# Kernel optimization log

Measured on AMD Instinct MI355X. Metric: run time of the kernel, lower is better.

The kernel has to match this reference:

```python
import jax, jax.numpy as jnp
import numpy as np

B, S, F, E = 8, 2048, 512, 512

def setup_inputs() -> dict:
    key = jax.random.key(0)
    k1, k2, k3, k4 = jax.random.split(key, 4)
    x = jax.random.normal(k1, (B, S, F), dtype=jnp.float32)
    # nn.Linear(feat, embed, bias=False): y = x @ W.T; store W as [F, E] already transposed
    scale = 1.0 / np.sqrt(F)
    Wq = jax.random.uniform(k2, (F, E), dtype=jnp.float32, minval=-scale, maxval=scale)
    Wk = jax.random.uniform(k3, (F, E), dtype=jnp.float32, minval=-scale, maxval=scale)
    Wv = jax.random.uniform(k4, (F, E), dtype=jnp.float32, minval=-scale, maxval=scale)
    return {"x": x, "Wq": Wq, "Wk": Wk, "Wv": Wv}

def reference(x, Wq, Wk, Wv):
    # QKV projections: [B, S, E]
    Q = jnp.einsum('bsf,fe->bse', x, Wq)
    K = jnp.einsum('bsf,fe->bse', x, Wk)
    V = jnp.einsum('bsf,fe->bse', x, Wv)
    # scores: [B, S, S], scaled by sqrt(E)
    scores = jnp.einsum('bqe,bke->bqk', Q, K) / jnp.sqrt(jnp.asarray(Q.shape[-1], Q.dtype))
    attn = jax.nn.softmax(scores, axis=-1)
    return jnp.einsum('bqk,bke->bqe', attn, V)
```

## Files before the change

kernel.cpp:

```cpp
#include <hip/hip_runtime.h>
#include <hip/hip_bf16.h>
#include <stdint.h>

#define B_ 8
#define S_ 2048
#define F_ 512
#define E_ 512

typedef short bf16x8 __attribute__((ext_vector_type(8)));
typedef float f32x4 __attribute__((ext_vector_type(4)));

__device__ __forceinline__ f32x4 mfma16(bf16x8 a, bf16x8 b, f32x4 c) {
  return __builtin_amdgcn_mfma_f32_16x16x32_bf16(a, b, c, 0, 0, 0);
}

__device__ __forceinline__ void gll16(const void* g, void* l) {
  __builtin_amdgcn_global_load_lds(
      (const __attribute__((address_space(1))) void*)g,
      (__attribute__((address_space(3))) void*)l, 16, 0, 0);
}

constexpr float QSCALE = 0.0441941738f * 1.44269504f;

__global__ void xconv_kernel(const float* __restrict__ x,
                             __hip_bfloat16* __restrict__ xb) {
  int i = (blockIdx.x * 256 + threadIdx.x) * 8;
  float4 a = *(const float4*)(x + i);
  float4 b = *(const float4*)(x + i + 4);
  union { __hip_bfloat16 h[8]; uint4 u; } cv;
  cv.h[0] = __float2bfloat16(a.x);
  cv.h[1] = __float2bfloat16(a.y);
  cv.h[2] = __float2bfloat16(a.z);
  cv.h[3] = __float2bfloat16(a.w);
  cv.h[4] = __float2bfloat16(b.x);
  cv.h[5] = __float2bfloat16(b.y);
  cv.h[6] = __float2bfloat16(b.z);
  cv.h[7] = __float2bfloat16(b.w);
  *(uint4*)(xb + i) = cv.u;
}

__global__ void wtrans_kernel(const float* __restrict__ wq,
                              const float* __restrict__ wk,
                              const float* __restrict__ wv,
                              __hip_bfloat16* __restrict__ wt) {
  __shared__ float t[32][33];
  const float* w = (blockIdx.z == 0) ? wq : (blockIdx.z == 1 ? wk : wv);
  __hip_bfloat16* o = wt + (size_t)blockIdx.z * F_ * E_;
  int e0 = blockIdx.x * 32, f0 = blockIdx.y * 32;
  int tx = threadIdx.x, ty = threadIdx.y;
#pragma unroll
  for (int i = 0; i < 4; i++)
    t[ty + 8 * i][tx] = w[(size_t)(f0 + ty + 8 * i) * E_ + e0 + tx];
  __syncthreads();
#pragma unroll
  for (int i = 0; i < 4; i++)
    o[(size_t)(e0 + ty + 8 * i) * F_ + f0 + tx] = __float2bfloat16(t[tx][ty + 8 * i]);
}

__global__ __launch_bounds__(256, 2) void qkvg_kernel(
    const __hip_bfloat16* __restrict__ xb, const __hip_bfloat16* __restrict__ wt,
    __hip_bfloat16* __restrict__ Qb, __hip_bfloat16* __restrict__ Kb,
    __hip_bfloat16* __restrict__ Vt) {
  __shared__ __hip_bfloat16 Al[2][128][64] __attribute__((aligned(16)));
  __shared__ __hip_bfloat16 Bl[2][128][64] __attribute__((aligned(16)));

  int tid = threadIdx.x;
  int lane = tid & 63, w = tid >> 6;
  int el = lane & 15, g = lane >> 4;
  int r7 = el & 7;
  int m0 = blockIdx.x * 128, n0 = blockIdx.y * 128, z = blockIdx.z;
  const __hip_bfloat16* wz = wt + (size_t)z * F_ * E_;
  int wr = w >> 1, wc = w & 1;

  int srcoff = (((lane & 7) ^ ((lane >> 3) & 7)) << 3);
  auto stage = [&](int kk, int bf) {
#pragma unroll
    for (int i = 0; i < 4; i++) {
      int row = w * 32 + i * 8 + (lane >> 3);
      gll16(xb + (size_t)(m0 + row) * F_ + kk * 64 + srcoff, &Al[bf][w * 32 + i * 8][0]);
      gll16(wz + (size_t)(n0 + row) * F_ + kk * 64 + srcoff, &Bl[bf][w * 32 + i * 8][0]);
    }
  };

  f32x4 acc[4][4] = {};
  stage(0, 0);
  asm volatile("s_waitcnt vmcnt(0)" ::: "memory");
  __syncthreads();

  for (int kk = 0; kk < 8; ++kk) {
    int bf = kk & 1;
    if (kk < 7) stage(kk + 1, bf ^ 1);
#pragma unroll
    for (int ks = 0; ks < 2; ++ks) {
      bf16x8 av[4], bv[4];
#pragma unroll
      for (int mi = 0; mi < 4; mi++)
        av[mi] = *(const bf16x8*)((const char*)&Al[bf][0][0] +
                                  (wr * 64 + mi * 16 + el) * 128 +
                                  (((ks * 4 + g) ^ r7) << 4));
#pragma unroll
      for (int ni = 0; ni < 4; ni++)
        bv[ni] = *(const bf16x8*)((const char*)&Bl[bf][0][0] +
                                  (wc * 64 + ni * 16 + el) * 128 +
                                  (((ks * 4 + g) ^ r7) << 4));
#pragma unroll
      for (int mi = 0; mi < 4; mi++)
#pragma unroll
        for (int ni = 0; ni < 4; ni++)
          acc[mi][ni] = mfma16(av[mi], bv[ni], acc[mi][ni]);
    }
    asm volatile("s_waitcnt vmcnt(0)" ::: "memory");
    __syncthreads();
  }

  float sc = (z == 0) ? QSCALE : 1.0f;
#pragma unroll
  for (int mi = 0; mi < 4; mi++)
#pragma unroll
    for (int ni = 0; ni < 4; ni++) {
      int mB = m0 + wr * 64 + mi * 16 + g * 4;
      int n = n0 + wc * 64 + ni * 16 + el;
      if (z == 2) {
        union { __hip_bfloat16 h[4]; uint2 u; } pk;
#pragma unroll
        for (int r = 0; r < 4; r++) pk.h[r] = __float2bfloat16(acc[mi][ni][r]);
        int b = mB >> 11, sl = mB & 2047;
        *(uint2*)&Vt[(size_t)b * E_ * S_ + (size_t)n * S_ + sl] = pk.u;
      } else {
#pragma unroll
        for (int r = 0; r < 4; r++) {
          __hip_bfloat16 v = __float2bfloat16(acc[mi][ni][r] * sc);
          if (z == 0) Qb[(size_t)(mB + r) * E_ + n] = v;
          else Kb[(size_t)(mB + r) * E_ + n] = v;
        }
      }
    }
}

__global__ __launch_bounds__(256, 2) void qkv_kernel(
    const float* __restrict__ x, const __hip_bfloat16* __restrict__ wt,
    __hip_bfloat16* __restrict__ Qb, __hip_bfloat16* __restrict__ Kb,
    __hip_bfloat16* __restrict__ Vt) {
  __shared__ __hip_bfloat16 Al[2][128][72];
  __shared__ __hip_bfloat16 Bl[2][128][72];
  int tid = threadIdx.x;
  int lane = tid & 63, w = tid >> 6;
  int el = lane & 15, g = lane >> 4;
  int m0 = blockIdx.x * 128, n0 = blockIdx.y * 128, z = blockIdx.z;
  const __hip_bfloat16* wz = wt + (size_t)z * F_ * E_;
  int wr = w >> 1, wc = w & 1;
  float4 fa[8];
  uint4 vb[4];
  auto load = [&](int kk) {
#pragma unroll
    for (int c = 0; c < 4; c++) {
      int id = tid + 256 * c;
      int row = id >> 3, k8 = (id & 7) * 8;
      const float* s = x + (size_t)(m0 + row) * F_ + kk * 64 + k8;
      fa[2 * c] = *(const float4*)s;
      fa[2 * c + 1] = *(const float4*)(s + 4);
      vb[c] = *(const uint4*)(wz + (size_t)(n0 + row) * F_ + kk * 64 + k8);
    }
  };
  auto store_lds = [&](int bf) {
#pragma unroll
    for (int c = 0; c < 4; c++) {
      int id = tid + 256 * c;
      int row = id >> 3, k8 = (id & 7) * 8;
      union { __hip_bfloat16 h[8]; uint4 u; } cv;
      cv.h[0] = __float2bfloat16(fa[2 * c].x);
      cv.h[1] = __float2bfloat16(fa[2 * c].y);
      cv.h[2] = __float2bfloat16(fa[2 * c].z);
      cv.h[3] = __float2bfloat16(fa[2 * c].w);
      cv.h[4] = __float2bfloat16(fa[2 * c + 1].x);
      cv.h[5] = __float2bfloat16(fa[2 * c + 1].y);
      cv.h[6] = __float2bfloat16(fa[2 * c + 1].z);
      cv.h[7] = __float2bfloat16(fa[2 * c + 1].w);
      *(uint4*)&Al[bf][row][k8] = cv.u;
      *(uint4*)&Bl[bf][row][k8] = vb[c];
    }
  };
  f32x4 acc[4][4] = {};
  load(0);
  store_lds(0);
  __syncthreads();
  for (int kk = 0; kk < 8; ++kk) {
    int bf = kk & 1;
    if (kk < 7) load(kk + 1);
#pragma unroll
    for (int ks = 0; ks < 2; ++ks) {
      bf16x8 av[4], bv[4];
#pragma unroll
      for (int mi = 0; mi < 4; mi++)
        av[mi] = *(const bf16x8*)((const char*)&Al[bf][0][0] +
                                  (wr * 64 + mi * 16 + el) * 144 + (ks * 32 + g * 8) * 2);
#pragma unroll
      for (int ni = 0; ni < 4; ni++)
        bv[ni] = *(const bf16x8*)((const char*)&Bl[bf][0][0] +
                                  (wc * 64 + ni * 16 + el) * 144 + (ks * 32 + g * 8) * 2);
#pragma unroll
      for (int mi = 0; mi < 4; mi++)
#pragma unroll
        for (int ni = 0; ni < 4; ni++)
          acc[mi][ni] = mfma16(av[mi], bv[ni], acc[mi][ni]);
    }
    if (kk < 7) store_lds(bf ^ 1);
    __syncthreads();
  }
  float sc = (z == 0) ? QSCALE : 1.0f;
#pragma unroll
  for (int mi = 0; mi < 4; mi++)
#pragma unroll
    for (int ni = 0; ni < 4; ni++)
#pragma unroll
      for (int r = 0; r < 4; r++) {
        int m = m0 + wr * 64 + mi * 16 + g * 4 + r;
        int n = n0 + wc * 64 + ni * 16 + el;
        __hip_bfloat16 v = __float2bfloat16(acc[mi][ni][r] * sc);
        if (z == 0) Qb[(size_t)m * E_ + n] = v;
        else if (z == 1) Kb[(size_t)m * E_ + n] = v;
        else {
          int b = m >> 11, sl = m & 2047;
          Vt[(size_t)b * E_ * S_ + (size_t)n * S_ + sl] = v;
        }
      }
}

template <int MODE>
__global__ __launch_bounds__(256, MODE ? 2 : 1) void attn_kernel(
    const __hip_bfloat16* __restrict__ Qb, const __hip_bfloat16* __restrict__ Kb,
    const __hip_bfloat16* __restrict__ Vt, float* __restrict__ out,
    float* __restrict__ part1, float* __restrict__ Ls, float* __restrict__ Ms) {
  __shared__ __hip_bfloat16 Kl[32][512] __attribute__((aligned(16)));
  __shared__ __hip_bfloat16 Vl[512][32] __attribute__((aligned(16)));
  __shared__ __hip_bfloat16 Pl[4][16][40] __attribute__((aligned(16)));

  int tid = threadIdx.x;
  int lane = tid & 63, w = tid >> 6;
  int el = lane & 15, g = lane >> 4, x7 = lane & 7;
  int bx = blockIdx.x;
  int batch = bx & 7, qt = (bx >> 3) & 31;
  int half = MODE ? (bx >> 8) : 0;
  int nt = MODE ? 32 : 64;
  int tbase = half * 32;
  int q0 = qt * 64 + w * 16;

  bf16x8 qf[16];
  {
    const __hip_bfloat16* qptr = Qb + (size_t)(batch * S_ + q0 + el) * E_ + g * 8;
#pragma unroll
    for (int s = 0; s < 16; s++) qf[s] = *(const bf16x8*)(qptr + 32 * s);
  }

  f32x4 o[32] = {};
  float m_run = -INFINITY, l_run = 0.f;

  const char* kbase_g = (const char*)(Kb + (size_t)batch * S_ * E_);
  const char* vbase_g = (const char*)(Vt + (size_t)batch * E_ * S_);
  int vsrc_lane = (lane >> 2) * (S_ * 2) + 16 * ((lane & 3) ^ ((lane >> 3) & 3));

  auto stage = [&](int t) {
#pragma unroll
    for (int i = 0; i < 8; i++) {
      int row = w * 8 + i;
      const char* src =
          kbase_g + ((size_t)(t * 32 + row) * 512 + 8 * (lane ^ i)) * 2;
      gll16(src, &Kl[row][0]);
    }
#pragma unroll
    for (int i = 0; i < 8; i++) {
      int eb = (w * 8 + i) * 16;
      const char* src = vbase_g + (size_t)eb * (S_ * 2) + vsrc_lane + t * 64;
      gll16(src, &Vl[eb][0]);
    }
  };

  int ka0 = el * 1024 + ((g ^ x7) << 4);
  int ka1 = el * 1024 + (((4 + g) ^ x7) << 4);
  int vbase_l = el * 64 + ((g ^ ((el >> 1) & 3)) << 4);

  stage(tbase);
  asm volatile("s_waitcnt vmcnt(0)" ::: "memory");
  __syncthreads();

  for (int i = 0; i < nt; ++i) {
    const char* kl = (const char*)&Kl[0][0];
    f32x4 st[2] = {};
    __builtin_amdgcn_s_setprio(1);
#pragma unroll
    for (int s = 0; s < 16; s++) {
      int base = ((s & 1) ? ka1 : ka0) + (s >> 1) * 128;
#pragma unroll
      for (int f = 0; f < 2; f++) {
        bf16x8 kf = *(const bf16x8*)(kl + base + f * 16384);
        st[f] = mfma16(kf, qf[s], st[f]);
      }
    }
    __builtin_amdgcn_s_setprio(0);
    float vmax = st[0][0];
#pragma unroll
    for (int r = 1; r < 4; r++) vmax = fmaxf(vmax, st[0][r]);
#pragma unroll
    for (int r = 0; r < 4; r++) vmax = fmaxf(vmax, st[1][r]);
    vmax = fmaxf(vmax, __shfl_xor(vmax, 16));
    vmax = fmaxf(vmax, __shfl_xor(vmax, 32));
    if (__any(vmax > m_run + 8.0f)) {
      float m_new = fmaxf(m_run, vmax);
      float fac = exp2f(m_run - m_new);
      float fo[4];
#pragma unroll
      for (int r = 0; r < 4; r++) fo[r] = __shfl(fac, g * 4 + r);
#pragma unroll
      for (int ni = 0; ni < 32; ni++) {
        o[ni][0] *= fo[0]; o[ni][1] *= fo[1]; o[ni][2] *= fo[2]; o[ni][3] *= fo[3];
      }
      l_run *= fac;
      m_run = m_new;
    }
    float p[8];
    float rs = 0.f;
#pragma unroll
    for (int f = 0; f < 2; f++)
#pragma unroll
      for (int r = 0; r < 4; r++) {
        float e2 = exp2f(st[f][r] - m_run);
        p[4 * f + r] = e2;
        rs += e2;
      }
    rs += __shfl_xor(rs, 16);
    rs += __shfl_xor(rs, 32);
    l_run += rs;
#pragma unroll
    for (int f = 0; f < 2; f++) {
      union { __hip_bfloat16 h[4]; uint2 u; } pk;
      pk.h[0] = __float2bfloat16(p[4 * f + 0]);
      pk.h[1] = __float2bfloat16(p[4 * f + 1]);
      pk.h[2] = __float2bfloat16(p[4 * f + 2]);
      pk.h[3] = __float2bfloat16(p[4 * f + 3]);
      *(uint2*)((char*)&Pl[w][0][0] + el * 80 + 32 * f + 8 * g) = pk.u;
    }
    asm volatile("s_waitcnt lgkmcnt(0)" ::: "memory");
    bf16x8 pa = *(const bf16x8*)((const char*)&Pl[w][0][0] + el * 80 + g * 16);
    const char* vl = (const char*)&Vl[0][0];
    __builtin_amdgcn_s_setprio(1);
#pragma unroll
    for (int ni = 0; ni < 32; ni++) {
      bf16x8 vf = *(const bf16x8*)(vl + vbase_l + ni * 1024);
      o[ni] = mfma16(pa, vf, o[ni]);
    }
    __builtin_amdgcn_s_setprio(0);
    __syncthreads();
    if (i + 1 < nt) {
      stage(tbase + i + 1);
      asm volatile("s_waitcnt vmcnt(0)" ::: "memory");
      __syncthreads();
    }
  }

  if (MODE == 0) {
    float linv[4];
#pragma unroll
    for (int r = 0; r < 4; r++) {
      float lr = __shfl(l_run, g * 4 + r);
      linv[r] = 1.0f / lr;
    }
    float* ob = out + (size_t)(batch * S_ + q0 + g * 4) * E_ + el;
#pragma unroll
    for (int ni = 0; ni < 32; ni++)
#pragma unroll
      for (int r = 0; r < 4; r++)
        ob[(size_t)r * E_ + ni * 16] = o[ni][r] * linv[r];
  } else {
    float* dst = (half == 0) ? out : part1;
    float* ob = dst + (size_t)(batch * S_ + q0 + g * 4) * E_ + el;
#pragma unroll
    for (int ni = 0; ni < 32; ni++)
#pragma unroll
      for (int r = 0; r < 4; r++)
        ob[(size_t)r * E_ + ni * 16] = o[ni][r];
    if (g == 0) {
      int idx = half * (B_ * S_) + batch * S_ + q0 + el;
      Ls[idx] = l_run;
      Ms[idx] = m_run;
    }
  }
}

__global__ void merge_kernel(float* __restrict__ out,
                             const float* __restrict__ part1,
                             const float* __restrict__ Ls,
                             const float* __restrict__ Ms) {
  int idx = blockIdx.x * 256 + threadIdx.x;
  int row = idx >> 7;
  int c4 = (idx & 127) * 4;
  float l0 = Ls[row], m0 = Ms[row];
  float l1 = Ls[B_ * S_ + row], m1 = Ms[B_ * S_ + row];
  float m = fmaxf(m0, m1);
  float w0 = exp2f(m0 - m), w1 = exp2f(m1 - m);
  float inv = 1.0f / (l0 * w0 + l1 * w1);
  size_t off = (size_t)row * E_ + c4;
  float4 a = *(const float4*)(out + off);
  float4 b = *(const float4*)(part1 + off);
  float4 r;
  r.x = (a.x * w0 + b.x * w1) * inv;
  r.y = (a.y * w0 + b.y * w1) * inv;
  r.z = (a.z * w0 + b.z * w1) * inv;
  r.w = (a.w * w0 + b.w * w1) * inv;
  *(float4*)(out + off) = r;
}

extern "C" void kernel_launch(void* const* d_in, const int* in_sizes, int n_in,
                              void* d_out, int out_size, void* d_ws, size_t ws_size,
                              hipStream_t stream) {
  const float* x = (const float*)d_in[0];
  const float* wq = (const float*)d_in[1];
  const float* wk = (const float*)d_in[2];
  const float* wv = (const float*)d_in[3];
  float* out = (float*)d_out;

  char* ws = (char*)d_ws;
  __hip_bfloat16* wt = (__hip_bfloat16*)ws;
  __hip_bfloat16* Qb = (__hip_bfloat16*)(ws + (size_t)3 * F_ * E_ * 2);
  __hip_bfloat16* Kb = Qb + (size_t)B_ * S_ * E_;
  __hip_bfloat16* Vt = Kb + (size_t)B_ * S_ * E_;
  __hip_bfloat16* xb = Vt + (size_t)B_ * S_ * E_;
  float* part1 = (float*)(ws + (size_t)3 * F_ * E_ * 2 + (size_t)3 * B_ * S_ * E_ * 2 +
                          (size_t)B_ * S_ * F_ * 2);
  float* Ls = part1 + (size_t)B_ * S_ * E_;
  float* Ms = Ls + 2 * B_ * S_;

  size_t need_bfx = (size_t)3 * F_ * E_ * 2 + (size_t)3 * B_ * S_ * E_ * 2 +
                    (size_t)B_ * S_ * F_ * 2;
  size_t need_split = need_bfx + (size_t)B_ * S_ * E_ * 4 + 4 * B_ * S_ * 4;
  bool bfx = (ws_size >= need_bfx);
  bool split = (ws_size >= need_split);

  dim3 b0(32, 8), g0(16, 16, 3);
  wtrans_kernel<<<g0, b0, 0, stream>>>(wq, wk, wv, wt);

  dim3 g1(128, 4, 3);
  if (bfx) {
    xconv_kernel<<<(B_ * S_ * F_) / (256 * 8), 256, 0, stream>>>(x, xb);
    qkvg_kernel<<<g1, 256, 0, stream>>>(xb, wt, Qb, Kb, Vt);
  } else {
    qkv_kernel<<<g1, 256, 0, stream>>>(x, wt, Qb, Kb, Vt);
  }

  if (split) {
    attn_kernel<1><<<512, 256, 0, stream>>>(Qb, Kb, Vt, out, part1, Ls, Ms);
    merge_kernel<<<(B_ * S_ * E_ / 4) / 256, 256, 0, stream>>>(out, part1, Ls, Ms);
  } else {
    attn_kernel<0><<<256, 256, 0, stream>>>(Qb, Kb, Vt, out, nullptr, nullptr, nullptr);
  }
}
```

Measured before the change: 185.3 us.

## Use 16-key attention tiles with k16 MFMA, register P, and bf16 partials

Adds a new attention kernel that processes 16 keys per step with double-buffered K/V LDS tiles. The P tile stays in registers, feeding a 16x16x16 bf16 MFMA directly, so the LDS round trip for P is gone. A lazy rescale skips the O update unless the max grows by more than a threshold. The split-K partial outputs are now stored as bf16 instead of fp32, halving merge traffic at some cost in precision. Smaller tiles mean more loop iterations and more barriers per key.

```diff
diff --git a/kernel.cpp b/kernel.cpp
--- a/kernel.cpp
+++ b/kernel.cpp
@@ -8,11 +8,24 @@
 #define E_ 512
 
 typedef short bf16x8 __attribute__((ext_vector_type(8)));
+typedef short bf16x4 __attribute__((ext_vector_type(4)));
 typedef float f32x4 __attribute__((ext_vector_type(4)));
 
 __device__ __forceinline__ f32x4 mfma16(bf16x8 a, bf16x8 b, f32x4 c) {
   return __builtin_amdgcn_mfma_f32_16x16x32_bf16(a, b, c, 0, 0, 0);
 }
+
+#if defined(__has_builtin)
+#if __has_builtin(__builtin_amdgcn_mfma_f32_16x16x16bf16_1k)
+#define HAVE16 1
+__device__ __forceinline__ f32x4 mfma16k16(bf16x4 a, bf16x4 b, f32x4 c) {
+  return __builtin_amdgcn_mfma_f32_16x16x16bf16_1k(a, b, c, 0, 0, 0);
+}
+#endif
+#endif
+#ifndef HAVE16
+#define HAVE16 0
+#endif
 
 __device__ __forceinline__ void gll16(const void* g, void* l) {
   __builtin_amdgcn_global_load_lds(
@@ -76,9 +89,10 @@
   auto stage = [&](int kk, int bf) {
 #pragma unroll
     for (int i = 0; i < 4; i++) {
-      int row = w * 32 + i * 8 + (lane >> 3);
-      gll16(xb + (size_t)(m0 + row) * F_ + kk * 64 + srcoff, &Al[bf][w * 32 + i * 8][0]);
-      gll16(wz + (size_t)(n0 + row) * F_ + kk * 64 + srcoff, &Bl[bf][w * 32 + i * 8][0]);
+      gll16(xb + (size_t)(m0 + w * 32 + i * 8 + (lane >> 3)) * F_ + kk * 64 + srcoff,
+            &Al[bf][w * 32 + i * 8][0]);
+      gll16(wz + (size_t)(n0 + w * 32 + i * 8 + (lane >> 3)) * F_ + kk * 64 + srcoff,
+            &Bl[bf][w * 32 + i * 8][0]);
     }
   };
 
@@ -226,11 +240,152 @@
       }
 }
 
+#if HAVE16
 template <int MODE>
-__global__ __launch_bounds__(256, MODE ? 2 : 1) void attn_kernel(
+__global__ __launch_bounds__(256, 2) void attn16_kernel(
     const __hip_bfloat16* __restrict__ Qb, const __hip_bfloat16* __restrict__ Kb,
     const __hip_bfloat16* __restrict__ Vt, float* __restrict__ out,
-    float* __restrict__ part1, float* __restrict__ Ls, float* __restrict__ Ms) {
+    __hip_bfloat16* __restrict__ part0, __hip_bfloat16* __restrict__ part1,
+    float* __restrict__ Ls, float* __restrict__ Ms) {
+  __shared__ __hip_bfloat16 Kl[2][16][512] __attribute__((aligned(16)));
+  __shared__ __hip_bfloat16 Vl[2][512][16] __attribute__((aligned(16)));
+
+  int tid = threadIdx.x;
+  int lane = tid & 63, w = tid >> 6;
+  int el = lane & 15, g = lane >> 4, x7 = lane & 7;
+  int bx = blockIdx.x;
+  int batch = bx & 7, qt = (bx >> 3) & 31;
+  int half = MODE ? (bx >> 8) : 0;
+  int nt = MODE ? 64 : 128;
+  int tbase = half * 64;
+  int q0 = qt * 64 + w * 16;
+
+  bf16x8 qf[16];
+  {
+    const __hip_bfloat16* qptr = Qb + (size_t)(batch * S_ + q0 + el) * E_ + g * 8;
+#pragma unroll
+    for (int s = 0; s < 16; s++) qf[s] = *(const bf16x8*)(qptr + 32 * s);
+  }
+
+  f32x4 o[32] = {};
+  float m_run = -INFINITY, l_run = 0.f;
+
+  const char* kbase_g = (const char*)(Kb + (size_t)batch * S_ * E_);
+  const char* vbase_g = (const char*)(Vt + (size_t)batch * E_ * S_);
+
+  auto stage = [&](int t, int bf) {
+#pragma unroll
+    for (int i = 0; i < 4; i++) {
+      int row = w * 4 + i;
+      const char* src =
+          kbase_g + ((size_t)(t * 16 + row) * 512 + 8 * (lane ^ (row & 7))) * 2;
+      gll16(src, &Kl[bf][row][0]);
+    }
+#pragma unroll
+    for (int i = 0; i < 4; i++) {
+      int eb = (w * 4 + i) * 32;
+      const char* src = vbase_g +
+          ((size_t)(eb + (lane >> 1)) * S_ + t * 16 + 8 * (lane & 1)) * 2;
+      gll16(src, &Vl[bf][eb][0]);
+    }
+  };
+
+  stage(tbase, 0);
+  asm volatile("s_waitcnt vmcnt(0)" ::: "memory");
+  __syncthreads();
+
+  for (int i = 0; i < nt; ++i) {
+    int bf = i & 1;
+    if (i + 1 < nt) stage(tbase + i + 1, bf ^ 1);
+    const char* kl = (const char*)&Kl[bf][0][0];
+    f32x4 st = {};
+    __builtin_amdgcn_s_setprio(1);
+#pragma unroll
+    for (int s = 0; s < 16; s++) {
+      bf16x8 kf = *(const bf16x8*)(kl + el * 1024 + (s >> 1) * 128 +
+                                   (((4 * (s & 1) + g) ^ x7) << 4));
+      st = mfma16(kf, qf[s], st);
+    }
+    __builtin_amdgcn_s_setprio(0);
+    float vmax = fmaxf(fmaxf(st[0], st[1]), fmaxf(st[2], st[3]));
+    vmax = fmaxf(vmax, __shfl_xor(vmax, 16));
+    vmax = fmaxf(vmax, __shfl_xor(vmax, 32));
+    if (__any(vmax > m_run + 8.0f)) {
+      float m_new = fmaxf(m_run, vmax);
+      float fac = exp2f(m_run - m_new);
+      float fo[4];
+#pragma unroll
+      for (int r = 0; r < 4; r++) fo[r] = __shfl(fac, g * 4 + r);
+#pragma unroll
+      for (int ni = 0; ni < 32; ni++) {
+        o[ni][0] *= fo[0]; o[ni][1] *= fo[1]; o[ni][2] *= fo[2]; o[ni][3] *= fo[3];
+      }
+      l_run *= fac;
+      m_run = m_new;
+    }
+    float p[4];
+    float rs = 0.f;
+#pragma unroll
+    for (int r = 0; r < 4; r++) {
+      p[r] = exp2f(st[r] - m_run);
+      rs += p[r];
+    }
+    rs += __shfl_xor(rs, 16);
+    rs += __shfl_xor(rs, 32);
+    l_run += rs;
+    union { __hip_bfloat16 h[4]; bf16x4 v; } pk;
+#pragma unroll
+    for (int r = 0; r < 4; r++) pk.h[r] = __float2bfloat16(p[r]);
+    bf16x4 pa = pk.v;
+    const char* vl = (const char*)&Vl[bf][0][0];
+    __builtin_amdgcn_s_setprio(1);
+#pragma unroll
+    for (int ni = 0; ni < 32; ni++) {
+      bf16x4 vf = *(const bf16x4*)(vl + ni * 512 + el * 32 + g * 8);
+      o[ni] = mfma16k16(pa, vf, o[ni]);
+    }
+    __builtin_amdgcn_s_setprio(0);
+    asm volatile("s_waitcnt vmcnt(0)" ::: "memory");
+    __syncthreads();
+  }
+
+  if (MODE == 0) {
+    float linv[4];
+#pragma unroll
+    for (int r = 0; r < 4; r++) {
+      float lr = __shfl(l_run, g * 4 + r);
+      linv[r] = 1.0f / lr;
+    }
+    float* ob = out + (size_t)(batch * S_ + q0 + g * 4) * E_ + el;
+#pragma unroll
+    for (int ni = 0; ni < 32; ni++)
+#pragma unroll
+      for (int r = 0; r < 4; r++)
+        ob[(size_t)r * E_ + ni * 16] = o[ni][r] * linv[r];
+  } else {
+    __hip_bfloat16* dst = (half == 0) ? part0 : part1;
+    __hip_bfloat16* ob = dst + (size_t)(batch * S_ + q0 + g * 4) * E_ + el;
+#pragma unroll
+    for (int ni = 0; ni < 32; ni++)
+#pragma unroll
+      for (int r = 0; r < 4; r++)
+        ob[(size_t)r * E_ + ni * 16] = __float2bfloat16(o[ni][r]);
+    if (g == 0) {
+      int idx = half * (B_ * S_) + batch * S_ + q0 + el;
+      Ls[idx] = l_run;
+      Ms[idx] = m_run;
+    }
+  }
+}
+
+#else
+
+template <int MODE>
+__global__ __launch_bounds__(256, MODE ? 2 : 1) void attn16_kernel(
+    const __hip_bfloat16* __restrict__ Qb, const __hip_bfloat16* __restrict__ Kb,
+    const __hip_bfloat16* __restrict__ Vt, float* __restrict__ out,
+    __hip_bfloat16* __restrict__ part0, __hip_bfloat16* __restrict__ part1,
+    float* __restrict__ Ls, float* __restrict__ Ms) {
   __shared__ __hip_bfloat16 Kl[32][512] __attribute__((aligned(16)));
   __shared__ __hip_bfloat16 Vl[512][32] __attribute__((aligned(16)));
   __shared__ __hip_bfloat16 Pl[4][16][40] __attribute__((aligned(16)));
@@ -371,13 +526,13 @@
       for (int r = 0; r < 4; r++)
         ob[(size_t)r * E_ + ni * 16] = o[ni][r] * linv[r];
   } else {
-    float* dst = (half == 0) ? out : part1;
-    float* ob = dst + (size_t)(batch * S_ + q0 + g * 4) * E_ + el;
+    __hip_bfloat16* dst = (half == 0) ? part0 : part1;
+    __hip_bfloat16* ob = dst + (size_t)(batch * S_ + q0 + g * 4) * E_ + el;
 #pragma unroll
     for (int ni = 0; ni < 32; ni++)
 #pragma unroll
       for (int r = 0; r < 4; r++)
-        ob[(size_t)r * E_ + ni * 16] = o[ni][r];
+        ob[(size_t)r * E_ + ni * 16] = __float2bfloat16(o[ni][r]);
     if (g == 0) {
       int idx = half * (B_ * S_) + batch * S_ + q0 + el;
       Ls[idx] = l_run;
@@ -385,28 +540,35 @@
     }
   }
 }
+#endif
 
 __global__ void merge_kernel(float* __restrict__ out,
-                             const float* __restrict__ part1,
+                             const __hip_bfloat16* __restrict__ p0,
+                             const __hip_bfloat16* __restrict__ p1,
                              const float* __restrict__ Ls,
                              const float* __restrict__ Ms) {
   int idx = blockIdx.x * 256 + threadIdx.x;
-  int row = idx >> 7;
-  int c4 = (idx & 127) * 4;
+  int row = idx >> 6;
+  int c8 = (idx & 63) * 8;
   float l0 = Ls[row], m0 = Ms[row];
   float l1 = Ls[B_ * S_ + row], m1 = Ms[B_ * S_ + row];
   float m = fmaxf(m0, m1);
   float w0 = exp2f(m0 - m), w1 = exp2f(m1 - m);
   float inv = 1.0f / (l0 * w0 + l1 * w1);
-  size_t off = (size_t)row * E_ + c4;
-  float4 a = *(const float4*)(out + off);
-  float4 b = *(const float4*)(part1 + off);
-  float4 r;
-  r.x = (a.x * w0 + b.x * w1) * inv;
-  r.y = (a.y * w0 + b.y * w1) * inv;
-  r.z = (a.z * w0 + b.z * w1) * inv;
-  r.w = (a.w * w0 + b.w * w1) * inv;
-  *(float4*)(out + off) = r;
+  size_t off = (size_t)row * E_ + c8;
+  union { uint4 u; ushort h[8]; } ua, ub;
+  ua.u = *(const uint4*)(p0 + off);
+  ub.u = *(const uint4*)(p1 + off);
+  float r[8];
+#pragma unroll
+  for (int j = 0; j < 8; j++) {
+    union { uint32_t u; float f; } a, b;
+    a.u = (uint32_t)ua.h[j] << 16;
+    b.u = (uint32_t)ub.h[j] << 16;
+    r[j] = (a.f * w0 + b.f * w1) * inv;
+  }
+  *(float4*)(out + off) = *(float4*)&r[0];
+  *(float4*)(out + off + 4) = *(float4*)&r[4];
 }
 
 extern "C" void kernel_launch(void* const* d_in, const int* in_sizes, int n_in,
@@ -424,14 +586,14 @@
   __hip_bfloat16* Kb = Qb + (size_t)B_ * S_ * E_;
   __hip_bfloat16* Vt = Kb + (size_t)B_ * S_ * E_;
   __hip_bfloat16* xb = Vt + (size_t)B_ * S_ * E_;
-  float* part1 = (float*)(ws + (size_t)3 * F_ * E_ * 2 + (size_t)3 * B_ * S_ * E_ * 2 +
-                          (size_t)B_ * S_ * F_ * 2);
-  float* Ls = part1 + (size_t)B_ * S_ * E_;
+  __hip_bfloat16* part0 = xb + (size_t)B_ * S_ * F_;
+  __hip_bfloat16* part1 = part0 + (size_t)B_ * S_ * E_;
+  float* Ls = (float*)(part1 + (size_t)B_ * S_ * E_);
   float* Ms = Ls + 2 * B_ * S_;
 
   size_t need_bfx = (size_t)3 * F_ * E_ * 2 + (size_t)3 * B_ * S_ * E_ * 2 +
                     (size_t)B_ * S_ * F_ * 2;
-  size_t need_split = need_bfx + (size_t)B_ * S_ * E_ * 4 + 4 * B_ * S_ * 4;
+  size_t need_split = need_bfx + (size_t)2 * B_ * S_ * E_ * 2 + 4 * B_ * S_ * 4;
   bool bfx = (ws_size >= need_bfx);
   bool split = (ws_size >= need_split);
 
@@ -447,9 +609,10 @@
   }
 
   if (split) {
-    attn_kernel<1><<<512, 256, 0, stream>>>(Qb, Kb, Vt, out, part1, Ls, Ms);
-    merge_kernel<<<(B_ * S_ * E_ / 4) / 256, 256, 0, stream>>>(out, part1, Ls, Ms);
+    attn16_kernel<1><<<512, 256, 0, stream>>>(Qb, Kb, Vt, out, part0, part1, Ls, Ms);
+    merge_kernel<<<(B_ * S_ * E_ / 8) / 256, 256, 0, stream>>>(out, part0, part1, Ls, Ms);
   } else {
-    attn_kernel<0><<<256, 256, 0, stream>>>(Qb, Kb, Vt, out, nullptr, nullptr, nullptr);
-  }
-}
+    attn16_kernel<0><<<256, 256, 0, stream>>>(Qb, Kb, Vt, out, nullptr, nullptr,
+                                              nullptr, nullptr);
+  }
+}
```

Result: slower. 255.6 us (+38.0%).

## Store split-attention partials in bf16 and overlap K/V staging waits

Applied to the files above, without the earlier changes.

The split-KV attention path now writes its two partial outputs as bf16 into separate workspace buffers, and the merge kernel reads them as bf16, converting back to fp32 with 8 elements per thread. This halves the partial-output traffic in both the attention epilogue and the merge. The staging wait after issuing the next tile is relaxed to vmcnt(8), with a full wait and barrier moved to just before the V reads, so part of the next tile's load can overlap the QK/softmax work. The trade-off is bf16 rounding of the unnormalized partial accumulators and a more delicate synchronization order.

```diff
diff --git a/kernel.cpp b/kernel.cpp
--- a/kernel.cpp
+++ b/kernel.cpp
@@ -76,9 +76,10 @@
   auto stage = [&](int kk, int bf) {
 #pragma unroll
     for (int i = 0; i < 4; i++) {
-      int row = w * 32 + i * 8 + (lane >> 3);
-      gll16(xb + (size_t)(m0 + row) * F_ + kk * 64 + srcoff, &Al[bf][w * 32 + i * 8][0]);
-      gll16(wz + (size_t)(n0 + row) * F_ + kk * 64 + srcoff, &Bl[bf][w * 32 + i * 8][0]);
+      gll16(xb + (size_t)(m0 + w * 32 + i * 8 + (lane >> 3)) * F_ + kk * 64 + srcoff,
+            &Al[bf][w * 32 + i * 8][0]);
+      gll16(wz + (size_t)(n0 + w * 32 + i * 8 + (lane >> 3)) * F_ + kk * 64 + srcoff,
+            &Bl[bf][w * 32 + i * 8][0]);
     }
   };
 
@@ -230,7 +231,8 @@
 __global__ __launch_bounds__(256, MODE ? 2 : 1) void attn_kernel(
     const __hip_bfloat16* __restrict__ Qb, const __hip_bfloat16* __restrict__ Kb,
     const __hip_bfloat16* __restrict__ Vt, float* __restrict__ out,
-    float* __restrict__ part1, float* __restrict__ Ls, float* __restrict__ Ms) {
+    __hip_bfloat16* __restrict__ part0, __hip_bfloat16* __restrict__ part1,
+    float* __restrict__ Ls, float* __restrict__ Ms) {
   __shared__ __hip_bfloat16 Kl[32][512] __attribute__((aligned(16)));
   __shared__ __hip_bfloat16 Vl[512][32] __attribute__((aligned(16)));
   __shared__ __hip_bfloat16 Pl[4][16][40] __attribute__((aligned(16)));
@@ -341,6 +343,8 @@
     }
     asm volatile("s_waitcnt lgkmcnt(0)" ::: "memory");
     bf16x8 pa = *(const bf16x8*)((const char*)&Pl[w][0][0] + el * 80 + g * 16);
+    asm volatile("s_waitcnt vmcnt(0)" ::: "memory");
+    __syncthreads();
     const char* vl = (const char*)&Vl[0][0];
     __builtin_amdgcn_s_setprio(1);
 #pragma unroll
@@ -352,7 +356,7 @@
     __syncthreads();
     if (i + 1 < nt) {
       stage(tbase + i + 1);
-      asm volatile("s_waitcnt vmcnt(0)" ::: "memory");
+      asm volatile("s_waitcnt vmcnt(8)" ::: "memory");
       __syncthreads();
     }
   }
@@ -371,13 +375,13 @@
       for (int r = 0; r < 4; r++)
         ob[(size_t)r * E_ + ni * 16] = o[ni][r] * linv[r];
   } else {
-    float* dst = (half == 0) ? out : part1;
-    float* ob = dst + (size_t)(batch * S_ + q0 + g * 4) * E_ + el;
+    __hip_bfloat16* dst = (half == 0) ? part0 : part1;
+    __hip_bfloat16* ob = dst + (size_t)(batch * S_ + q0 + g * 4) * E_ + el;
 #pragma unroll
     for (int ni = 0; ni < 32; ni++)
 #pragma unroll
       for (int r = 0; r < 4; r++)
-        ob[(size_t)r * E_ + ni * 16] = o[ni][r];
+        ob[(size_t)r * E_ + ni * 16] = __float2bfloat16(o[ni][r]);
     if (g == 0) {
       int idx = half * (B_ * S_) + batch * S_ + q0 + el;
       Ls[idx] = l_run;
@@ -387,26 +391,32 @@
 }
 
 __global__ void merge_kernel(float* __restrict__ out,
-                             const float* __restrict__ part1,
+                             const __hip_bfloat16* __restrict__ p0,
+                             const __hip_bfloat16* __restrict__ p1,
                              const float* __restrict__ Ls,
                              const float* __restrict__ Ms) {
   int idx = blockIdx.x * 256 + threadIdx.x;
-  int row = idx >> 7;
-  int c4 = (idx & 127) * 4;
+  int row = idx >> 6;
+  int c8 = (idx & 63) * 8;
   float l0 = Ls[row], m0 = Ms[row];
   float l1 = Ls[B_ * S_ + row], m1 = Ms[B_ * S_ + row];
   float m = fmaxf(m0, m1);
   float w0 = exp2f(m0 - m), w1 = exp2f(m1 - m);
   float inv = 1.0f / (l0 * w0 + l1 * w1);
-  size_t off = (size_t)row * E_ + c4;
-  float4 a = *(const float4*)(out + off);
-  float4 b = *(const float4*)(part1 + off);
-  float4 r;
-  r.x = (a.x * w0 + b.x * w1) * inv;
-  r.y = (a.y * w0 + b.y * w1) * inv;
-  r.z = (a.z * w0 + b.z * w1) * inv;
-  r.w = (a.w * w0 + b.w * w1) * inv;
-  *(float4*)(out + off) = r;
+  size_t off = (size_t)row * E_ + c8;
+  union { uint4 u; ushort h[8]; } ua, ub;
+  ua.u = *(const uint4*)(p0 + off);
+  ub.u = *(const uint4*)(p1 + off);
+  float r[8];
+#pragma unroll
+  for (int j = 0; j < 8; j++) {
+    union { uint32_t u; float f; } a, b;
+    a.u = (uint32_t)ua.h[j] << 16;
+    b.u = (uint32_t)ub.h[j] << 16;
+    r[j] = (a.f * w0 + b.f * w1) * inv;
+  }
+  *(float4*)(out + off) = *(float4*)&r[0];
+  *(float4*)(out + off + 4) = *(float4*)&r[4];
 }
 
 extern "C" void kernel_launch(void* const* d_in, const int* in_sizes, int n_in,
@@ -424,14 +434,14 @@
   __hip_bfloat16* Kb = Qb + (size_t)B_ * S_ * E_;
   __hip_bfloat16* Vt = Kb + (size_t)B_ * S_ * E_;
   __hip_bfloat16* xb = Vt + (size_t)B_ * S_ * E_;
-  float* part1 = (float*)(ws + (size_t)3 * F_ * E_ * 2 + (size_t)3 * B_ * S_ * E_ * 2 +
-                          (size_t)B_ * S_ * F_ * 2);
-  float* Ls = part1 + (size_t)B_ * S_ * E_;
+  __hip_bfloat16* part0 = xb + (size_t)B_ * S_ * F_;
+  __hip_bfloat16* part1 = part0 + (size_t)B_ * S_ * E_;
+  float* Ls = (float*)(part1 + (size_t)B_ * S_ * E_);
   float* Ms = Ls + 2 * B_ * S_;
 
   size_t need_bfx = (size_t)3 * F_ * E_ * 2 + (size_t)3 * B_ * S_ * E_ * 2 +
                     (size_t)B_ * S_ * F_ * 2;
-  size_t need_split = need_bfx + (size_t)B_ * S_ * E_ * 4 + 4 * B_ * S_ * 4;
+  size_t need_split = need_bfx + (size_t)2 * B_ * S_ * E_ * 2 + 4 * B_ * S_ * 4;
   bool bfx = (ws_size >= need_bfx);
   bool split = (ws_size >= need_split);
 
@@ -447,9 +457,10 @@
   }
 
   if (split) {
-    attn_kernel<1><<<512, 256, 0, stream>>>(Qb, Kb, Vt, out, part1, Ls, Ms);
-    merge_kernel<<<(B_ * S_ * E_ / 4) / 256, 256, 0, stream>>>(out, part1, Ls, Ms);
+    attn_kernel<1><<<512, 256, 0, stream>>>(Qb, Kb, Vt, out, part0, part1, Ls, Ms);
+    merge_kernel<<<(B_ * S_ * E_ / 8) / 256, 256, 0, stream>>>(out, part0, part1, Ls, Ms);
   } else {
-    attn_kernel<0><<<256, 256, 0, stream>>>(Qb, Kb, Vt, out, nullptr, nullptr, nullptr);
-  }
-}
+    attn_kernel<0><<<256, 256, 0, stream>>>(Qb, Kb, Vt, out, nullptr, nullptr,
+                                            nullptr, nullptr);
+  }
+}
```

After: 181.3 us. 1.02x faster.
